# Kernel optimization log

Measured on AMD Instinct MI355X. Metric: run time of the kernel, lower is better.

Reference implementation:

```python
import jax, jax.numpy as jnp
import numpy as np


def _conv1d(x, w, b, stride, pad):
    # x: [N, C_in, L], w: [C_out, C_in, K]
    out = jax.lax.conv_general_dilated(
        x, w, window_strides=(stride,), padding=[(pad, pad)],
        dimension_numbers=("NCH", "OIH", "NCH"))
    return out + b[None, :, None]


def _maxpool1d(x, k, stride, pad):
    return jax.lax.reduce_window(
        x, -jnp.inf, jax.lax.max,
        window_dimensions=(1, 1, k), window_strides=(1, 1, stride),
        padding=[(0, 0), (0, 0), (pad, pad)])


def setup_inputs() -> dict:
    key = jax.random.key(0)
    ks = jax.random.split(key, 9)
    bs, n_nodes, T = 256, 128, 1216
    irep = (32, 64, 128)
    s = 0.05
    return {
        "x": jax.random.normal(ks[0], (bs, n_nodes, T), dtype=jnp.float32),
        "w1": jax.random.normal(ks[1], (irep[0], 1, 10), dtype=jnp.float32) * s,
        "b1": jax.random.normal(ks[2], (irep[0],), dtype=jnp.float32) * s,
        "w2": jax.random.normal(ks[3], (irep[1], irep[0], 3), dtype=jnp.float32) * s,
        "b2": jax.random.normal(ks[4], (irep[1],), dtype=jnp.float32) * s,
        "w3": jax.random.normal(ks[5], (irep[2], irep[1], 4), dtype=jnp.float32) * s,
        "b3": jax.random.normal(ks[6], (irep[2],), dtype=jnp.float32) * s,
        "wl": jax.random.normal(ks[7], (3, n_nodes * irep[2]), dtype=jnp.float32) * s,
        "bl": jax.random.normal(ks[8], (3,), dtype=jnp.float32) * s,
    }


def reference(x, w1, b1, w2, b2, w3, b3, wl, bl):
    bs, n_nodes, T = x.shape
    # nodes are independent per-stage -> fold node dim into batch (batches
    # the original per-node Python loop into single convs per stage)
    h = x.reshape(bs * n_nodes, 1, T)
    h = jax.nn.relu(_conv1d(h, w1, b1, stride=8, pad=1))   # [BN, irep0, 152]
    h = jax.nn.relu(_maxpool1d(h, 5, 5, 0))                # [BN, irep0, 30]
    h = jax.nn.relu(_conv1d(h, w2, b2, stride=3, pad=0))   # [BN, irep1, 10]
    h = jax.nn.relu(_maxpool1d(h, 3, 3, 1))                # [BN, irep1, 4]
    h = jax.nn.relu(_conv1d(h, w3, b3, stride=1, pad=0))   # [BN, irep2, 1]
    feat = h.reshape(bs, n_nodes * w3.shape[0])            # [bs, n_nodes*irep2]
    logits = feat @ wl.T + bl                              # [bs, 3]
    return jax.nn.softmax(logits, axis=1)
```

## Files before the change

### kernel.cpp

```cpp
#include <hip/hip_runtime.h>
#include <math.h>


typedef __attribute__((ext_vector_type(8))) short bf16x8;
typedef __attribute__((ext_vector_type(4))) float f32x4;

__device__ __forceinline__ ushort f2bf(float f) {
    union { float f; uint u; } c; c.f = f;
    return (ushort)((c.u + 0x7FFFu + ((c.u >> 16) & 1u)) >> 16);
}

#define S2  264
#define XPS 136
#define H1S 104

__global__ void k0_prep(const float* __restrict__ w2, ushort* __restrict__ w2b,
                        const float* __restrict__ w3, ushort* __restrict__ w3b,
                        const float* __restrict__ w1, ushort* __restrict__ w1b) {
    int i = blockIdx.x * 256 + threadIdx.x;
    if (i < 6144) {
        int c = i / 96, r = i - c * 96;
        int ci = r / 3, d = r - ci * 3;
        w2b[c * 96 + d * 32 + ci] = f2bf(w2[i]);
    }
    int j = i - 6144;
    if (j >= 0 && j < 32768) w3b[j] = f2bf(w3[j]);
    int j3 = i - 38912;
    if (j3 >= 0 && j3 < 1024) {
        int H = j3 >> 9, r9 = j3 & 511, c = r9 >> 5, k = r9 & 31;
        int ch = H * 16 + c;
        ushort val = 0;
        if (k >= 3 && k <= 12) {
            val = (ushort)(__float_as_uint(w1[ch * 10 + k - 3]) >> 16);
        } else if (k >= 19 && k <= 28) {
            float w = w1[ch * 10 + k - 19];
            float hf = __uint_as_float(__float_as_uint(w) & 0xFFFF0000u);
            val = f2bf(w - hf);
        }
        w1b[j3] = val;
    }
}

__global__ __launch_bounds__(256) void k_fused(
    const float* __restrict__ x,
    const float* __restrict__ b1,
    const ushort* __restrict__ w2b,
    const float* __restrict__ b2,
    const ushort* __restrict__ w3b,
    const float* __restrict__ b3,
    const float* __restrict__ wl,
    float* __restrict__ partials)
{
    __shared__ __align__(16) ushort arena[4][6016];
    __shared__ float red[4][3];
    const int wave = threadIdx.x >> 6, lane = threadIdx.x & 63;
    const int lm   = lane & 15, quad = lane >> 4, qm = quad & 1;
    const int bn0  = blockIdx.x * 64 + wave * 16;
    const float* xw0 = x + (size_t)bn0 * 1216;

    ushort* hp  = arena[wave];
    ushort* lp  = hp + 16 * XPS;
    ushort* h1t = lp + 16 * XPS;

    const ushort* w1b = w2b + 6144;
    const bf16x8 wA0 = *(const bf16x8*)(w1b + lm * 32 + quad * 8);
    const bf16x8 wA1 = *(const bf16x8*)(w1b + 512 + lm * 32 + quad * 8);
    const f32x4  b1i0 = *(const f32x4*)(b1 + quad * 4);
    const f32x4  b1i1 = *(const f32x4*)(b1 + 16 + quad * 4);
    float bias2[4];
    #pragma unroll
    for (int nt = 0; nt < 4; ++nt) bias2[nt] = b2[nt * 16 + lm];

    f32x4 cur[4];
    #pragma unroll
    for (int nt = 0; nt < 4; ++nt) cur[nt] = (f32x4){-3e38f,-3e38f,-3e38f,-3e38f};
    uint2 pk[4][4];

    for (int q = 0; q < 10; ++q) {
        const int fq = 120 * q - 4;
        #pragma unroll
        for (int j = 0; j < 8; ++j) {
            const int idx = lane + 64 * j;
            const int row = idx >> 5, c4 = idx & 31;
            const int off = fq + 4 * c4;
            const float* src = xw0 + (size_t)row * 1216 + (off < 0 ? 0 : off);
            float4 v = *(const float4*)src;
            if (off < 0) v.w = 0.f;
            const uint ux = __float_as_uint(v.x), uy = __float_as_uint(v.y);
            const uint uz = __float_as_uint(v.z), uw = __float_as_uint(v.w);
            ushort4 hs = make_ushort4((ushort)(ux >> 16), (ushort)(uy >> 16),
                                      (ushort)(uz >> 16), (ushort)(uw >> 16));
            const float lx = v.x - __uint_as_float(ux & 0xFFFF0000u);
            const float ly = v.y - __uint_as_float(uy & 0xFFFF0000u);
            const float lz = v.z - __uint_as_float(uz & 0xFFFF0000u);
            const float lw = v.w - __uint_as_float(uw & 0xFFFF0000u);
            ushort4 ls = make_ushort4((ushort)(__float_as_uint(lx) >> 16),
                                      (ushort)(__float_as_uint(ly) >> 16),
                                      (ushort)(__float_as_uint(lz) >> 16),
                                      (ushort)(__float_as_uint(lw) >> 16));
            *(ushort4*)&hp[row * XPS + 4 * c4] = hs;
            *(ushort4*)&lp[row * XPS + 4 * c4] = ls;
        }

        #pragma unroll
        for (int tw = 0; tw < 3; ++tw) {
            f32x4 mx0 = (f32x4){0.f,0.f,0.f,0.f};
            f32x4 mx1 = (f32x4){0.f,0.f,0.f,0.f};
            #pragma unroll
            for (int ts = 0; ts < 5; ++ts) {
                const int tl = 5 * tw + ts;
                const int jb = 8 * tl + 8 * qm;
                bf16x8 bh = *(const bf16x8*)(hp + lm * XPS + jb);
                bf16x8 bl = *(const bf16x8*)(lp + lm * XPS + jb);
                f32x4 a0 = __builtin_amdgcn_mfma_f32_16x16x32_bf16(wA0, bh, b1i0, 0, 0, 0);
                a0 = __builtin_amdgcn_mfma_f32_16x16x32_bf16(wA0, bl, a0, 0, 0, 0);
                f32x4 a1 = __builtin_amdgcn_mfma_f32_16x16x32_bf16(wA1, bh, b1i1, 0, 0, 0);
                a1 = __builtin_amdgcn_mfma_f32_16x16x32_bf16(wA1, bl, a1, 0, 0, 0);
                #pragma unroll
                for (int r = 0; r < 4; ++r) {
                    mx0[r] = fmaxf(mx0[r], a0[r]);
                    mx1[r] = fmaxf(mx1[r], a1[r]);
                }
            }
            ushort4 p0, p1;
            p0.x = f2bf(mx0[0]); p0.y = f2bf(mx0[1]);
            p0.z = f2bf(mx0[2]); p0.w = f2bf(mx0[3]);
            p1.x = f2bf(mx1[0]); p1.y = f2bf(mx1[1]);
            p1.z = f2bf(mx1[2]); p1.w = f2bf(mx1[3]);
            *(ushort4*)&h1t[lm * H1S + 32 * tw + quad * 4]      = p0;
            *(ushort4*)&h1t[lm * H1S + 32 * tw + 16 + quad * 4] = p1;
        }

        f32x4 acc[4];
        #pragma unroll
        for (int nt = 0; nt < 4; ++nt) acc[nt] = (f32x4){0.f,0.f,0.f,0.f};
        #pragma unroll
        for (int kc = 0; kc < 3; ++kc) {
            bf16x8 afv = *(const bf16x8*)&h1t[lm * H1S + 32 * kc + quad * 8];
            #pragma unroll
            for (int nt = 0; nt < 4; ++nt) {
                bf16x8 bfr = *(const bf16x8*)(w2b + (nt*16 + lm)*96 + kc*32 + quad*8);
                acc[nt] = __builtin_amdgcn_mfma_f32_16x16x32_bf16(afv, bfr, acc[nt], 0, 0, 0);
            }
        }

        const bool fresh = (q == 0 || q == 2 || q == 5 || q == 8);
        #pragma unroll
        for (int nt = 0; nt < 4; ++nt)
            #pragma unroll
            for (int r = 0; r < 4; ++r)
                cur[nt][r] = fresh ? acc[nt][r] : fmaxf(cur[nt][r], acc[nt][r]);

        if (q == 1 || q == 4 || q == 7 || q == 9) {
            const int w = (q == 1) ? 0 : (q == 4) ? 1 : (q == 7) ? 2 : 3;
            #pragma unroll
            for (int nt = 0; nt < 4; ++nt)
                #pragma unroll
                for (int r = 0; r < 4; ++r) {
                    float f = fmaxf(cur[nt][r] + bias2[nt], 0.f);
                    uint hb = (uint)f2bf(f);
                    if (w == 0)      pk[nt][r].x  = hb;
                    else if (w == 1) pk[nt][r].x |= hb << 16;
                    else if (w == 2) pk[nt][r].y  = hb;
                    else             pk[nt][r].y |= hb << 16;
                }
        }
    }

    ushort* shw = arena[wave];
    #pragma unroll
    for (int nt = 0; nt < 4; ++nt)
        #pragma unroll
        for (int r = 0; r < 4; ++r)
            *(uint2*)(shw + (quad*4 + r) * S2 + (nt*16 + lm) * 4) = pk[nt][r];

    bf16x8 afr[8];
    #pragma unroll
    for (int kc = 0; kc < 8; ++kc)
        afr[kc] = *(const bf16x8*)(shw + lm * S2 + kc * 32 + quad * 8);

    const int node0 = bn0 & 127;
    const float* wlr = wl + (node0 + quad * 4) * 128 + lm;
    float a0 = 0.f, a1 = 0.f, a2 = 0.f;
    for (int nt3 = 0; nt3 < 8; ++nt3) {
        f32x4 acc3 = (f32x4){0.f, 0.f, 0.f, 0.f};
        const ushort* bb = w3b + (size_t)(nt3 * 16 + lm) * 256 + quad * 8;
        #pragma unroll
        for (int kc = 0; kc < 8; ++kc) {
            bf16x8 bf3 = *(const bf16x8*)(bb + kc * 32);
            acc3 = __builtin_amdgcn_mfma_f32_16x16x32_bf16(afr[kc], bf3, acc3, 0, 0, 0);
        }
        const float b3v = b3[nt3 * 16 + lm];
        #pragma unroll
        for (int r = 0; r < 4; ++r) {
            float f = fmaxf(acc3[r] + b3v, 0.f);
            const float* wp = wlr + r * 128 + nt3 * 16;
            a0 = fmaf(f, wp[0],     a0);
            a1 = fmaf(f, wp[16384], a1);
            a2 = fmaf(f, wp[32768], a2);
        }
    }

    #pragma unroll
    for (int off = 32; off > 0; off >>= 1) {
        a0 += __shfl_xor(a0, off);
        a1 += __shfl_xor(a1, off);
        a2 += __shfl_xor(a2, off);
    }
    if (lane == 0) { red[wave][0] = a0; red[wave][1] = a1; red[wave][2] = a2; }
    __syncthreads();
    if (threadIdx.x < 3) {
        float s = red[0][threadIdx.x] + red[1][threadIdx.x]
                + red[2][threadIdx.x] + red[3][threadIdx.x];
        partials[blockIdx.x * 3 + threadIdx.x] = s;
    }
}

__global__ void k_soft(const float* __restrict__ partials,
                       const float* __restrict__ bl,
                       float* __restrict__ out) {
    const int b = threadIdx.x;
    float l0 = partials[(2*b)*3+0] + partials[(2*b+1)*3+0] + bl[0];
    float l1 = partials[(2*b)*3+1] + partials[(2*b+1)*3+1] + bl[1];
    float l2 = partials[(2*b)*3+2] + partials[(2*b+1)*3+2] + bl[2];
    float m  = fmaxf(l0, fmaxf(l1, l2));
    float e0 = expf(l0 - m), e1 = expf(l1 - m), e2 = expf(l2 - m);
    float s  = e0 + e1 + e2;
    out[b*3+0] = e0 / s; out[b*3+1] = e1 / s; out[b*3+2] = e2 / s;
}

extern "C" void kernel_launch(void* const* d_in, const int* in_sizes, int n_in,
                              void* d_out, int out_size, void* d_ws, size_t ws_size,
                              hipStream_t stream) {
    const float* x  = (const float*)d_in[0];
    const float* w1 = (const float*)d_in[1];
    const float* b1 = (const float*)d_in[2];
    const float* w2 = (const float*)d_in[3];
    const float* b2 = (const float*)d_in[4];
    const float* w3 = (const float*)d_in[5];
    const float* b3 = (const float*)d_in[6];
    const float* wl = (const float*)d_in[7];
    const float* bl = (const float*)d_in[8];
    float* out = (float*)d_out;

    ushort* w2b      = (ushort*)d_ws;
    ushort* w1b      = w2b + 6144;
    ushort* w3b      = (ushort*)((char*)d_ws + 16384);
    float*  partials = (float*)((char*)d_ws + 16384 + 65536);

    k0_prep<<<156, 256, 0, stream>>>(w2, w2b, w3, w3b, w1, w1b);
    k_fused<<<512, 256, 0, stream>>>(x, b1, w2b, b2, w3b, b3, wl, partials);
    k_soft<<<1, 256, 0, stream>>>(partials, bl, out);
}
```

Before: 257.3 us.

## Fuse weight prep and softmax into main kernel with last-block reduction

Removes the separate weight-conversion and softmax kernels. Each block now converts w1 and w2 to bf16 in shared memory (w2 with a padded stride), converts w3 from fp32 to bf16 on the fly inside the stage-3 MFMA loop, and uses an atomic counter so the last block to finish computes the softmax. This trades two kernel launches for a memset and some redundant per-block conversion work, plus doubled w3 global traffic per block.

Result: slower. 282.7 us (+9.8%).

```diff
diff --git a/kernel.cpp b/kernel.cpp
--- a/kernel.cpp
+++ b/kernel.cpp
@@ -13,21 +13,40 @@
 #define S2  264
 #define XPS 136
 #define H1S 104
-
-__global__ void k0_prep(const float* __restrict__ w2, ushort* __restrict__ w2b,
-                        const float* __restrict__ w3, ushort* __restrict__ w3b,
-                        const float* __restrict__ w1, ushort* __restrict__ w1b) {
-    int i = blockIdx.x * 256 + threadIdx.x;
-    if (i < 6144) {
+#define W2S 104
+
+__global__ __launch_bounds__(256) void k_fused(
+    const float* __restrict__ x,
+    const float* __restrict__ w1,
+    const float* __restrict__ b1,
+    const float* __restrict__ w2,
+    const float* __restrict__ b2,
+    const float* __restrict__ w3,
+    const float* __restrict__ b3,
+    const float* __restrict__ wl,
+    const float* __restrict__ blg,
+    float* __restrict__ partials,
+    uint*  __restrict__ cnt,
+    float* __restrict__ out)
+{
+    __shared__ __align__(16) ushort arena[4][6016];
+    __shared__ __align__(16) ushort w2bL[64 * W2S];
+    __shared__ __align__(16) ushort w1bL[1024];
+    __shared__ float red[4][3];
+    __shared__ int sh_last;
+    const int tid  = threadIdx.x;
+    const int wave = tid >> 6, lane = tid & 63;
+    const int lm   = lane & 15, quad = lane >> 4, qm = quad & 1;
+    const int bn0  = blockIdx.x * 64 + wave * 16;
+    const float* xw0 = x + (size_t)bn0 * 1216;
+
+    for (int i = tid; i < 6144; i += 256) {
         int c = i / 96, r = i - c * 96;
         int ci = r / 3, d = r - ci * 3;
-        w2b[c * 96 + d * 32 + ci] = f2bf(w2[i]);
-    }
-    int j = i - 6144;
-    if (j >= 0 && j < 32768) w3b[j] = f2bf(w3[j]);
-    int j3 = i - 38912;
-    if (j3 >= 0 && j3 < 1024) {
-        int H = j3 >> 9, r9 = j3 & 511, c = r9 >> 5, k = r9 & 31;
+        w2bL[c * W2S + d * 32 + ci] = f2bf(w2[i]);
+    }
+    for (int i = tid; i < 1024; i += 256) {
+        int H = i >> 9, r9 = i & 511, c = r9 >> 5, k = r9 & 31;
         int ch = H * 16 + c;
         ushort val = 0;
         if (k >= 3 && k <= 12) {
@@ -37,34 +56,16 @@
             float hf = __uint_as_float(__float_as_uint(w) & 0xFFFF0000u);
             val = f2bf(w - hf);
         }
-        w1b[j3] = val;
-    }
-}
-
-__global__ __launch_bounds__(256) void k_fused(
-    const float* __restrict__ x,
-    const float* __restrict__ b1,
-    const ushort* __restrict__ w2b,
-    const float* __restrict__ b2,
-    const ushort* __restrict__ w3b,
-    const float* __restrict__ b3,
-    const float* __restrict__ wl,
-    float* __restrict__ partials)
-{
-    __shared__ __align__(16) ushort arena[4][6016];
-    __shared__ float red[4][3];
-    const int wave = threadIdx.x >> 6, lane = threadIdx.x & 63;
-    const int lm   = lane & 15, quad = lane >> 4, qm = quad & 1;
-    const int bn0  = blockIdx.x * 64 + wave * 16;
-    const float* xw0 = x + (size_t)bn0 * 1216;
+        w1bL[i] = val;
+    }
+    __syncthreads();
 
     ushort* hp  = arena[wave];
     ushort* lp  = hp + 16 * XPS;
     ushort* h1t = lp + 16 * XPS;
 
-    const ushort* w1b = w2b + 6144;
-    const bf16x8 wA0 = *(const bf16x8*)(w1b + lm * 32 + quad * 8);
-    const bf16x8 wA1 = *(const bf16x8*)(w1b + 512 + lm * 32 + quad * 8);
+    const bf16x8 wA0 = *(const bf16x8*)(w1bL + lm * 32 + quad * 8);
+    const bf16x8 wA1 = *(const bf16x8*)(w1bL + 512 + lm * 32 + quad * 8);
     const f32x4  b1i0 = *(const f32x4*)(b1 + quad * 4);
     const f32x4  b1i1 = *(const f32x4*)(b1 + 16 + quad * 4);
     float bias2[4];
@@ -139,7 +140,7 @@
             bf16x8 afv = *(const bf16x8*)&h1t[lm * H1S + 32 * kc + quad * 8];
             #pragma unroll
             for (int nt = 0; nt < 4; ++nt) {
-                bf16x8 bfr = *(const bf16x8*)(w2b + (nt*16 + lm)*96 + kc*32 + quad*8);
+                bf16x8 bfr = *(const bf16x8*)(w2bL + (nt*16 + lm)*W2S + kc*32 + quad*8);
                 acc[nt] = __builtin_amdgcn_mfma_f32_16x16x32_bf16(afv, bfr, acc[nt], 0, 0, 0);
             }
         }
@@ -184,11 +185,17 @@
     float a0 = 0.f, a1 = 0.f, a2 = 0.f;
     for (int nt3 = 0; nt3 < 8; ++nt3) {
         f32x4 acc3 = (f32x4){0.f, 0.f, 0.f, 0.f};
-        const ushort* bb = w3b + (size_t)(nt3 * 16 + lm) * 256 + quad * 8;
+        const float* w3r = w3 + (size_t)(nt3 * 16 + lm) * 256 + quad * 8;
         #pragma unroll
         for (int kc = 0; kc < 8; ++kc) {
-            bf16x8 bf3 = *(const bf16x8*)(bb + kc * 32);
-            acc3 = __builtin_amdgcn_mfma_f32_16x16x32_bf16(afr[kc], bf3, acc3, 0, 0, 0);
+            float4 u0 = *(const float4*)(w3r + kc * 32);
+            float4 u1 = *(const float4*)(w3r + kc * 32 + 4);
+            union { ushort u[8]; bf16x8 v; } bf;
+            bf.u[0] = f2bf(u0.x); bf.u[1] = f2bf(u0.y);
+            bf.u[2] = f2bf(u0.z); bf.u[3] = f2bf(u0.w);
+            bf.u[4] = f2bf(u1.x); bf.u[5] = f2bf(u1.y);
+            bf.u[6] = f2bf(u1.z); bf.u[7] = f2bf(u1.w);
+            acc3 = __builtin_amdgcn_mfma_f32_16x16x32_bf16(afr[kc], bf.v, acc3, 0, 0, 0);
         }
         const float b3v = b3[nt3 * 16 + lm];
         #pragma unroll
@@ -209,24 +216,35 @@
     }
     if (lane == 0) { red[wave][0] = a0; red[wave][1] = a1; red[wave][2] = a2; }
     __syncthreads();
-    if (threadIdx.x < 3) {
-        float s = red[0][threadIdx.x] + red[1][threadIdx.x]
-                + red[2][threadIdx.x] + red[3][threadIdx.x];
-        partials[blockIdx.x * 3 + threadIdx.x] = s;
-    }
-}
-
-__global__ void k_soft(const float* __restrict__ partials,
-                       const float* __restrict__ bl,
-                       float* __restrict__ out) {
-    const int b = threadIdx.x;
-    float l0 = partials[(2*b)*3+0] + partials[(2*b+1)*3+0] + bl[0];
-    float l1 = partials[(2*b)*3+1] + partials[(2*b+1)*3+1] + bl[1];
-    float l2 = partials[(2*b)*3+2] + partials[(2*b+1)*3+2] + bl[2];
-    float m  = fmaxf(l0, fmaxf(l1, l2));
-    float e0 = expf(l0 - m), e1 = expf(l1 - m), e2 = expf(l2 - m);
-    float s  = e0 + e1 + e2;
-    out[b*3+0] = e0 / s; out[b*3+1] = e1 / s; out[b*3+2] = e2 / s;
+
+    if (tid < 3) {
+        float s = red[0][tid] + red[1][tid] + red[2][tid] + red[3][tid];
+        __hip_atomic_store(&partials[blockIdx.x * 3 + tid], s,
+                           __ATOMIC_RELEASE, __HIP_MEMORY_SCOPE_AGENT);
+    }
+    __syncthreads();
+    if (tid == 0) {
+        uint old = __hip_atomic_fetch_add(cnt, 1u, __ATOMIC_ACQ_REL,
+                                          __HIP_MEMORY_SCOPE_AGENT);
+        sh_last = (old == 511u);
+    }
+    __syncthreads();
+
+    if (sh_last) {
+        const int b = tid;
+        float l0 = blg[0], l1 = blg[1], l2 = blg[2];
+        #pragma unroll
+        for (int j = 0; j < 2; ++j) {
+            const float* pr = partials + (2 * b + j) * 3;
+            l0 += __hip_atomic_load(pr + 0, __ATOMIC_ACQUIRE, __HIP_MEMORY_SCOPE_AGENT);
+            l1 += __hip_atomic_load(pr + 1, __ATOMIC_ACQUIRE, __HIP_MEMORY_SCOPE_AGENT);
+            l2 += __hip_atomic_load(pr + 2, __ATOMIC_ACQUIRE, __HIP_MEMORY_SCOPE_AGENT);
+        }
+        float m  = fmaxf(l0, fmaxf(l1, l2));
+        float e0 = expf(l0 - m), e1 = expf(l1 - m), e2 = expf(l2 - m);
+        float s  = e0 + e1 + e2;
+        out[b*3+0] = e0 / s; out[b*3+1] = e1 / s; out[b*3+2] = e2 / s;
+    }
 }
 
 extern "C" void kernel_launch(void* const* d_in, const int* in_sizes, int n_in,
@@ -243,12 +261,10 @@
     const float* bl = (const float*)d_in[8];
     float* out = (float*)d_out;
 
-    ushort* w2b      = (ushort*)d_ws;
-    ushort* w1b      = w2b + 6144;
-    ushort* w3b      = (ushort*)((char*)d_ws + 16384);
-    float*  partials = (float*)((char*)d_ws + 16384 + 65536);
-
-    k0_prep<<<156, 256, 0, stream>>>(w2, w2b, w3, w3b, w1, w1b);
-    k_fused<<<512, 256, 0, stream>>>(x, b1, w2b, b2, w3b, b3, wl, partials);
-    k_soft<<<1, 256, 0, stream>>>(partials, bl, out);
+    float* partials = (float*)d_ws;
+    uint*  cnt      = (uint*)((char*)d_ws + 8192);
+
+    hipMemsetAsync(cnt, 0, 4, stream);
+    k_fused<<<512, 256, 0, stream>>>(x, w1, b1, w2, b2, w3, b3, wl, bl,
+                                     partials, cnt, out);
 }
```

## Split each 16-row tile's time chunks and conv3 output tiles across two waves

Applied to the files above, without the earlier changes.

Each 16-row group of batch-node rows is now handled by a two-wave block instead of one wave. The two waves split the 10 time chunks of the conv1/pool/conv2 stage 5 and 5, exchange their packed pooled results through shared memory with barriers, then split the conv3 output tiles between them. The goal is to shorten each wave's serial dependency chain and raise the total wave count, improving latency hiding, at the cost of extra block syncs and four times as many partial sums for the softmax kernel to add up.

New measurement: 261.3 us. No clear change (+1.6%).

```diff
diff --git a/kernel.cpp b/kernel.cpp
--- a/kernel.cpp
+++ b/kernel.cpp
@@ -41,7 +41,7 @@
     }
 }
 
-__global__ __launch_bounds__(256) void k_fused(
+__global__ __launch_bounds__(128) void k_fused(
     const float* __restrict__ x,
     const float* __restrict__ b1,
     const ushort* __restrict__ w2b,
@@ -51,14 +51,15 @@
     const float* __restrict__ wl,
     float* __restrict__ partials)
 {
-    __shared__ __align__(16) ushort arena[4][6016];
-    __shared__ float red[4][3];
-    const int wave = threadIdx.x >> 6, lane = threadIdx.x & 63;
+    __shared__ __align__(16) ushort arena[2][6016];
+    __shared__ float red[2][3];
+    const int tid  = threadIdx.x;
+    const int h    = tid >> 6, lane = tid & 63;
     const int lm   = lane & 15, quad = lane >> 4, qm = quad & 1;
-    const int bn0  = blockIdx.x * 64 + wave * 16;
+    const int bn0  = blockIdx.x * 16;
     const float* xw0 = x + (size_t)bn0 * 1216;
 
-    ushort* hp  = arena[wave];
+    ushort* hp  = arena[h];
     ushort* lp  = hp + 16 * XPS;
     ushort* h1t = lp + 16 * XPS;
 
@@ -74,9 +75,10 @@
     f32x4 cur[4];
     #pragma unroll
     for (int nt = 0; nt < 4; ++nt) cur[nt] = (f32x4){-3e38f,-3e38f,-3e38f,-3e38f};
-    uint2 pk[4][4];
-
-    for (int q = 0; q < 10; ++q) {
+    uint pk[4][4];
+
+    for (int ql = 0; ql < 5; ++ql) {
+        const int q = 5 * h + ql;
         const int fq = 120 * q - 4;
         #pragma unroll
         for (int j = 0; j < 8; ++j) {
@@ -144,45 +146,47 @@
             }
         }
 
-        const bool fresh = (q == 0 || q == 2 || q == 5 || q == 8);
+        const bool fresh = (ql == 0) || (ql == 2 + h);
         #pragma unroll
         for (int nt = 0; nt < 4; ++nt)
             #pragma unroll
             for (int r = 0; r < 4; ++r)
                 cur[nt][r] = fresh ? acc[nt][r] : fmaxf(cur[nt][r], acc[nt][r]);
 
-        if (q == 1 || q == 4 || q == 7 || q == 9) {
-            const int w = (q == 1) ? 0 : (q == 4) ? 1 : (q == 7) ? 2 : 3;
+        if (ql == 1 + h || ql == 4) {
+            const int w = (ql == 4) ? 1 : 0;
             #pragma unroll
             for (int nt = 0; nt < 4; ++nt)
                 #pragma unroll
                 for (int r = 0; r < 4; ++r) {
                     float f = fmaxf(cur[nt][r] + bias2[nt], 0.f);
                     uint hb = (uint)f2bf(f);
-                    if (w == 0)      pk[nt][r].x  = hb;
-                    else if (w == 1) pk[nt][r].x |= hb << 16;
-                    else if (w == 2) pk[nt][r].y  = hb;
-                    else             pk[nt][r].y |= hb << 16;
+                    if (w == 0) pk[nt][r]  = hb;
+                    else        pk[nt][r] |= hb << 16;
                 }
         }
     }
 
-    ushort* shw = arena[wave];
+    __syncthreads();
+    ushort* sh2 = arena[0];
     #pragma unroll
     for (int nt = 0; nt < 4; ++nt)
         #pragma unroll
         for (int r = 0; r < 4; ++r)
-            *(uint2*)(shw + (quad*4 + r) * S2 + (nt*16 + lm) * 4) = pk[nt][r];
+            *(uint*)(sh2 + (quad*4 + r) * S2 + (nt*16 + lm) * 4 + 2 * h) = pk[nt][r];
+    __syncthreads();
 
     bf16x8 afr[8];
     #pragma unroll
     for (int kc = 0; kc < 8; ++kc)
-        afr[kc] = *(const bf16x8*)(shw + lm * S2 + kc * 32 + quad * 8);
+        afr[kc] = *(const bf16x8*)(sh2 + lm * S2 + kc * 32 + quad * 8);
 
     const int node0 = bn0 & 127;
     const float* wlr = wl + (node0 + quad * 4) * 128 + lm;
     float a0 = 0.f, a1 = 0.f, a2 = 0.f;
-    for (int nt3 = 0; nt3 < 8; ++nt3) {
+    #pragma unroll
+    for (int t3 = 0; t3 < 4; ++t3) {
+        const int nt3 = 4 * h + t3;
         f32x4 acc3 = (f32x4){0.f, 0.f, 0.f, 0.f};
         const ushort* bb = w3b + (size_t)(nt3 * 16 + lm) * 256 + quad * 8;
         #pragma unroll
@@ -207,12 +211,10 @@
         a1 += __shfl_xor(a1, off);
         a2 += __shfl_xor(a2, off);
     }
-    if (lane == 0) { red[wave][0] = a0; red[wave][1] = a1; red[wave][2] = a2; }
+    if (lane == 0) { red[h][0] = a0; red[h][1] = a1; red[h][2] = a2; }
     __syncthreads();
-    if (threadIdx.x < 3) {
-        float s = red[0][threadIdx.x] + red[1][threadIdx.x]
-                + red[2][threadIdx.x] + red[3][threadIdx.x];
-        partials[blockIdx.x * 3 + threadIdx.x] = s;
+    if (tid < 3) {
+        partials[blockIdx.x * 3 + tid] = red[0][tid] + red[1][tid];
     }
 }
 
@@ -220,9 +222,12 @@
                        const float* __restrict__ bl,
                        float* __restrict__ out) {
     const int b = threadIdx.x;
-    float l0 = partials[(2*b)*3+0] + partials[(2*b+1)*3+0] + bl[0];
-    float l1 = partials[(2*b)*3+1] + partials[(2*b+1)*3+1] + bl[1];
-    float l2 = partials[(2*b)*3+2] + partials[(2*b+1)*3+2] + bl[2];
+    float l0 = bl[0], l1 = bl[1], l2 = bl[2];
+    #pragma unroll
+    for (int j = 0; j < 8; ++j) {
+        const float* pr = partials + (8*b + j) * 3;
+        l0 += pr[0]; l1 += pr[1]; l2 += pr[2];
+    }
     float m  = fmaxf(l0, fmaxf(l1, l2));
     float e0 = expf(l0 - m), e1 = expf(l1 - m), e2 = expf(l2 - m);
     float s  = e0 + e1 + e2;
@@ -249,6 +254,6 @@
     float*  partials = (float*)((char*)d_ws + 16384 + 65536);
 
     k0_prep<<<156, 256, 0, stream>>>(w2, w2b, w3, w3b, w1, w1b);
-    k_fused<<<512, 256, 0, stream>>>(x, b1, w2b, b2, w3b, b3, wl, partials);
+    k_fused<<<2048, 128, 0, stream>>>(x, b1, w2b, b2, w3b, b3, wl, partials);
     k_soft<<<1, 256, 0, stream>>>(partials, bl, out);
 }
```
